# Optimization experiments

Hardware: AMD Instinct MI355X
Metric: run time of the kernel (lower is better)

## Reference

```python
import jax, jax.numpy as jnp
import numpy as np

N = 50000   # total nodes in batch
E = 640000  # directed edges
G = 64      # graphs in batch
D_IN = 128
D_H = 128
D_OUT = 10


def _glorot(key, shape):
    fan_in = shape[0]
    return jax.random.normal(key, shape, dtype=jnp.float32) / np.sqrt(fan_in)


def setup_inputs() -> dict:
    key = jax.random.key(0)
    ks = jax.random.split(key, 10)
    x = jax.random.normal(ks[0], (N, D_IN), dtype=jnp.float32)
    src = jax.random.randint(ks[1], (E,), 0, N, dtype=jnp.int32)
    dst = jax.random.randint(ks[2], (E,), 0, N, dtype=jnp.int32)
    batch = jnp.sort(jax.random.randint(ks[3], (N,), 0, G, dtype=jnp.int32))
    return {
        "x": x, "src": src, "dst": dst, "batch": batch,
        "W1": _glorot(ks[4], (D_IN, D_H)), "b1": jnp.zeros((D_H,), jnp.float32),
        "W2": _glorot(ks[5], (D_H, D_H)), "b2": jnp.zeros((D_H,), jnp.float32),
        "W3": _glorot(ks[6], (D_H, D_H)), "b3": jnp.zeros((D_H,), jnp.float32),
        "Wl": _glorot(ks[7], (D_H, D_OUT)), "bl": jnp.zeros((D_OUT,), jnp.float32),
    }


def gcn_conv(x, W, b, src, dst):
    """PyG GCNConv: add self-loops, symmetric deg^-1/2 normalization,
    linear transform, scatter-sum aggregation at dst, plus bias."""
    n = x.shape[0]
    loops = jnp.arange(n, dtype=src.dtype)
    s = jnp.concatenate([src, loops])  # [E+N]
    d = jnp.concatenate([dst, loops])
    deg = jax.ops.segment_sum(jnp.ones_like(d, dtype=x.dtype), d, num_segments=n)
    dinv = jnp.where(deg > 0, jax.lax.rsqrt(deg), 0.0)
    norm = dinv[s] * dinv[d]                        # [E+N]
    h = x @ W                                       # [N, D]
    out = jax.ops.segment_sum(h[s] * norm[:, None], d, num_segments=n)
    return out + b


def reference(x, src, dst, batch, W1, b1, W2, b2, W3, b3, Wl, bl):
    n = x.shape[0]
    h = jax.nn.relu(gcn_conv(x, W1, b1, src, dst))
    # dropout is a no-op in eval mode
    h = jax.nn.relu(gcn_conv(h, W2, b2, src, dst))
    h = gcn_conv(h, W3, b3, src, dst)
    # global_mean_pool over graph ids
    sums = jax.ops.segment_sum(h, batch, num_segments=G)            # [G, D]
    counts = jax.ops.segment_sum(jnp.ones((n,), h.dtype), batch, num_segments=G)
    pooled = sums / jnp.maximum(counts, 1.0)[:, None]
    logits = pooled @ Wl + bl                                       # [G, D_OUT]
    return jax.nn.log_softmax(logits, axis=1)
```

## Files before the change

kernel.cpp:

```cpp
#include <hip/hip_runtime.h>


constexpr int D = 128;
constexpr int DOUT = 10;
constexpr int PSPLIT = 8;
constexpr int BSH = 3;
constexpr int BCAP = 192;
constexpr int CPAD = 16;

using short8  = __attribute__((ext_vector_type(8))) short;
using float4v = __attribute__((ext_vector_type(4))) float;
using f32x2   = __attribute__((ext_vector_type(2))) float;

__device__ __forceinline__ ushort f2bf(float f) {
  uint u = __float_as_uint(f);
  return (ushort)((u + 0x7fffu + ((u >> 16) & 1u)) >> 16);
}
__device__ __forceinline__ float bfhi(uint u) { return __uint_as_float(u & 0xffff0000u); }


__global__ void init_kernel(int* __restrict__ bcnt, int total) {
  int i = blockIdx.x * blockDim.x + threadIdx.x;
  if (i < total) bcnt[i] = 0;
}

__global__ void binfill_kernel(const int* __restrict__ src, const int* __restrict__ dst,
    int* __restrict__ bcnt, uint* __restrict__ buck, int e) {
  int i = blockIdx.x * blockDim.x + threadIdx.x;
  if (i >= e) return;
  int d = dst[i], s = src[i];
  int b = d >> BSH;
  int pos = atomicAdd(&bcnt[b * CPAD], 1);
  if (pos < BCAP)
    buck[(size_t)b * BCAP + pos] = (uint)s | ((uint)(d & ((1 << BSH) - 1)) << 16);
}

__global__ __launch_bounds__(256) void countb_kernel(const uint* __restrict__ buck,
    const int* __restrict__ bcnt, int* __restrict__ cnt, float* __restrict__ dinv,
    int* __restrict__ bsum, int n) {
  __shared__ int lc[256];
  const int base = blockIdx.x * 256;
  const int m = min(256, n - base);
  lc[threadIdx.x] = 0;
  __syncthreads();
  const int b0 = base >> BSH;
  #pragma unroll
  for (int bb = 0; bb < (256 >> BSH); ++bb) {
    int b = b0 + bb;
    if ((b << BSH) >= n) break;
    int c = min(bcnt[b * CPAD], BCAP);
    for (int i = threadIdx.x; i < c; i += 256)
      atomicAdd(&lc[(bb << BSH) + (int)(buck[(size_t)b * BCAP + i] >> 16)], 1);
  }
  __syncthreads();
  int v = lc[threadIdx.x];
  if ((int)threadIdx.x < m) {
    cnt[base + threadIdx.x] = v;
    dinv[base + threadIdx.x] = rsqrtf((float)(v + 1));
  }
  __shared__ int sd[256];
  sd[threadIdx.x] = ((int)threadIdx.x < m) ? v : 0;
  __syncthreads();
  for (int off = 128; off > 0; off >>= 1) {
    if (threadIdx.x < (unsigned)off) sd[threadIdx.x] += sd[threadIdx.x + off];
    __syncthreads();
  }
  if (threadIdx.x == 0) bsum[blockIdx.x] = sd[0];
}

__global__ __launch_bounds__(1024) void scan2_kernel(const int* __restrict__ bsum,
    int* __restrict__ boff, int nb, int* __restrict__ rowptr, int n) {
  __shared__ int sd[1024];
  int v = ((int)threadIdx.x < nb) ? bsum[threadIdx.x] : 0;
  sd[threadIdx.x] = v;
  __syncthreads();
  for (int off = 1; off < 1024; off <<= 1) {
    int t = (threadIdx.x >= (unsigned)off) ? sd[threadIdx.x - off] : 0;
    __syncthreads();
    sd[threadIdx.x] += t;
    __syncthreads();
  }
  if ((int)threadIdx.x < nb) boff[threadIdx.x] = sd[threadIdx.x] - v;
  if ((int)threadIdx.x == nb - 1) rowptr[n] = sd[threadIdx.x];
}

__global__ __launch_bounds__(256) void scatter_kernel(const uint* __restrict__ buck,
    const int* __restrict__ bcnt, const int* __restrict__ cnt,
    const int* __restrict__ boff, int* __restrict__ rowptr,
    const float* __restrict__ dinv, uint* __restrict__ epk, int n) {
  __shared__ int sd[256];
  __shared__ int lcur[256];
  const int base = blockIdx.x * 256;
  const int i = base + (int)threadIdx.x;
  int v = (i < n) ? cnt[i] : 0;
  sd[threadIdx.x] = v;
  __syncthreads();
  for (int off = 1; off < 256; off <<= 1) {
    int t = (threadIdx.x >= (unsigned)off) ? sd[threadIdx.x - off] : 0;
    __syncthreads();
    sd[threadIdx.x] += t;
    __syncthreads();
  }
  int rp = boff[blockIdx.x] + sd[threadIdx.x] - v;
  if (i < n) {
    rowptr[i] = rp;
    lcur[threadIdx.x] = rp;
  }
  __syncthreads();
  const int b0 = base >> BSH;
  #pragma unroll
  for (int bb = 0; bb < (256 >> BSH); ++bb) {
    int b = b0 + bb;
    if ((b << BSH) >= n) break;
    int c = min(bcnt[b * CPAD], BCAP);
    for (int j = threadIdx.x; j < c; j += 256) {
      uint rec = buck[(size_t)b * BCAP + j];
      int dl = (int)(rec >> 16);
      int s = (int)(rec & 0xffffu);
      int d = (b << BSH) + dl;
      int slot = atomicAdd(&lcur[(bb << BSH) + dl], 1);
      epk[slot] = (uint)s | ((uint)f2bf(dinv[s] * dinv[d]) << 16);
    }
  }
}

__global__ __launch_bounds__(256) void prepw_kernel(const float* __restrict__ W1,
    const float* __restrict__ W2, const float* __restrict__ W3, ushort* __restrict__ Wp) {
  const float* W = (blockIdx.y == 0) ? W1 : (blockIdx.y == 1) ? W2 : W3;
  ushort* Wpo = Wp + (size_t)blockIdx.y * 2048 * 8;
  int idx = blockIdx.x * 256 + threadIdx.x;
  int cf = idx >> 8, kk = (idx >> 6) & 3, lane = idx & 63;
  int k0 = kk * 32 + (lane >> 4) * 8;
  int c = cf * 16 + (lane & 15);
  uint p[4];
  #pragma unroll
  for (int h = 0; h < 4; ++h) {
    ushort lo = f2bf(W[(k0 + 2 * h) * D + c]);
    ushort hi = f2bf(W[(k0 + 2 * h + 1) * D + c]);
    p[h] = (uint)lo | ((uint)hi << 16);
  }
  uint4 w = make_uint4(p[0], p[1], p[2], p[3]);
  *(uint4*)(Wpo + idx * 8) = w;
}

__global__ __launch_bounds__(256) void gemm_mfma(const float* __restrict__ Ain,
    const ushort* __restrict__ Wp, uchar* __restrict__ out, int n) {
  __shared__ ushort wl[2048 * 8];
  const int tid = threadIdx.x;
  #pragma unroll
  for (int i = 0; i < 8; ++i) {
    int idx = tid + i * 256;
    *(uint4*)(&wl[idx * 8]) = *(const uint4*)(Wp + idx * 8);
  }
  __syncthreads();
  const int w = tid >> 6, lane = tid & 63;
  const int row0 = blockIdx.x * 64 + w * 16;
  int arow = row0 + (lane & 15);
  if (arow >= n) arow = n - 1;

  short8 a[4];
  const float* abase = Ain + (size_t)arow * D + ((lane >> 4) * 8);
  #pragma unroll
  for (int kk = 0; kk < 4; ++kk) {
    float4 f0 = *(const float4*)(abase + kk * 32);
    float4 f1 = *(const float4*)(abase + kk * 32 + 4);
    short8 v;
    v[0] = (short)f2bf(f0.x); v[1] = (short)f2bf(f0.y);
    v[2] = (short)f2bf(f0.z); v[3] = (short)f2bf(f0.w);
    v[4] = (short)f2bf(f1.x); v[5] = (short)f2bf(f1.y);
    v[6] = (short)f2bf(f1.z); v[7] = (short)f2bf(f1.w);
    a[kk] = v;
  }

  float4v acc[8] = {};
  #pragma unroll
  for (int kk = 0; kk < 4; ++kk) {
    #pragma unroll
    for (int cf = 0; cf < 8; ++cf) {
      short8 b = *(const short8*)(&wl[((cf * 4 + kk) * 64 + lane) * 8]);
      acc[cf] = __builtin_amdgcn_mfma_f32_16x16x32_bf16(a[kk], b, acc[cf], 0, 0, 0);
    }
  }
  const int crow = row0 + (lane >> 4) * 4;
  const int ccol = lane & 15;
  #pragma unroll
  for (int cf = 0; cf < 8; ++cf) {
    #pragma unroll
    for (int r = 0; r < 4; ++r) {
      if (crow + r < n) {
        int enc = __builtin_amdgcn_cvt_pk_fp8_f32(acc[cf][r], acc[cf][r], 0, false);
        out[(size_t)(crow + r) * D + cf * 16 + ccol] = (uchar)(enc & 0xff);
      }
    }
  }
}

__device__ __forceinline__ void agg_node(const uchar* __restrict__ h8,
    const int* __restrict__ rowptr, const uint* __restrict__ epk,
    const float* __restrict__ dinv, const float* __restrict__ bias,
    int node, int sub, int li, int relu,
    float& a0, float& a1, float& a2, float& a3) {
  const int beg = rowptr[node], end = rowptr[node + 1];
  a0 = a1 = a2 = a3 = 0.f;
  for (int e = beg; e < end; e += 16) {
    uint mm[8], rr[8];
    #pragma unroll
    for (int k = 0; k < 8; ++k)
      mm[k] = epk[min(e + 2 * k + sub, end - 1)];
    #pragma unroll
    for (int k = 0; k < 8; ++k)
      rr[k] = *(const uint*)(h8 + (size_t)(mm[k] & 0xffffu) * D + li * 4);
    #pragma unroll
    for (int k = 0; k < 8; ++k) {
      float wk = (e + 2 * k + sub < end) ? bfhi(mm[k]) : 0.f;
      f32x2 pa = __builtin_amdgcn_cvt_pk_f32_fp8(rr[k], false);
      f32x2 pb = __builtin_amdgcn_cvt_pk_f32_fp8(rr[k], true);
      a0 += pa[0] * wk;
      a1 += pa[1] * wk;
      a2 += pb[0] * wk;
      a3 += pb[1] * wk;
    }
  }
  a0 += __shfl_xor(a0, 32);
  a1 += __shfl_xor(a1, 32);
  a2 += __shfl_xor(a2, 32);
  a3 += __shfl_xor(a3, 32);
  const float di = dinv[node];
  const float dsq = di * di;
  uint sv = *(const uint*)(h8 + (size_t)node * D + li * 4);
  f32x2 sa = __builtin_amdgcn_cvt_pk_f32_fp8(sv, false);
  f32x2 sb = __builtin_amdgcn_cvt_pk_f32_fp8(sv, true);
  a0 += sa[0] * dsq;
  a1 += sa[1] * dsq;
  a2 += sb[0] * dsq;
  a3 += sb[1] * dsq;
  float4 bv = *(const float4*)(bias + li * 4);
  a0 += bv.x; a1 += bv.y; a2 += bv.z; a3 += bv.w;
  if (relu) {
    a0 = fmaxf(a0, 0.f); a1 = fmaxf(a1, 0.f);
    a2 = fmaxf(a2, 0.f); a3 = fmaxf(a3, 0.f);
  }
}

__global__ __launch_bounds__(256) void aggemm_kernel(const uchar* __restrict__ h8,
    const int* __restrict__ rowptr, const uint* __restrict__ epk,
    const float* __restrict__ dinv, const float* __restrict__ bias,
    const ushort* __restrict__ Wp, uchar* __restrict__ out8, int n) {
  __shared__ ushort At[16][136];
  const int wv = (int)(threadIdx.x >> 6);
  const int lane = (int)(threadIdx.x & 63);
  const int sub = lane >> 5;
  const int li = lane & 31;
  const int node0 = blockIdx.x * 16;
  #pragma unroll
  for (int t = 0; t < 4; ++t) {
    const int row = wv * 4 + t;
    const int node = node0 + row;
    if (node < n) {
      float a0, a1, a2, a3;
      agg_node(h8, rowptr, epk, dinv, bias, node, sub, li, 1, a0, a1, a2, a3);
      if (sub == 0) {
        uint2 pk;
        pk.x = (uint)f2bf(a0) | ((uint)f2bf(a1) << 16);
        pk.y = (uint)f2bf(a2) | ((uint)f2bf(a3) << 16);
        *(uint2*)(&At[row][li * 4]) = pk;
      }
    } else if (sub == 0) {
      *(uint2*)(&At[row][li * 4]) = make_uint2(0, 0);
    }
  }
  __syncthreads();
  const int r = lane & 15;
  const int koff = (lane >> 4) * 8;
  short8 a[4];
  #pragma unroll
  for (int kk = 0; kk < 4; ++kk)
    a[kk] = *(const short8*)(&At[r][koff + kk * 32]);
  const int crow = node0 + (lane >> 4) * 4;
  const int ccol = lane & 15;
  #pragma unroll
  for (int cc = 0; cc < 2; ++cc) {
    const int cf = wv * 2 + cc;
    float4v acc = {};
    #pragma unroll
    for (int kk = 0; kk < 4; ++kk) {
      short8 b = *(const short8*)(Wp + (size_t)((cf * 4 + kk) * 64 + lane) * 8);
      acc = __builtin_amdgcn_mfma_f32_16x16x32_bf16(a[kk], b, acc, 0, 0, 0);
    }
    #pragma unroll
    for (int r2 = 0; r2 < 4; ++r2) {
      if (crow + r2 < n) {
        int enc = __builtin_amdgcn_cvt_pk_fp8_f32(acc[r2], acc[r2], 0, false);
        out8[(size_t)(crow + r2) * D + cf * 16 + ccol] = (uchar)(enc & 0xff);
      }
    }
  }
}

__global__ __launch_bounds__(256) void agg_kernel(const uchar* __restrict__ h8,
    const int* __restrict__ rowptr, const uint* __restrict__ epk,
    const float* __restrict__ dinv, const float* __restrict__ bias,
    uchar* __restrict__ out8, int n, int relu) {
  int node = (int)((blockIdx.x * blockDim.x + threadIdx.x) >> 6);
  if (node >= n) return;
  const int lane = threadIdx.x & 63;
  const int sub = lane >> 5;
  const int li = lane & 31;
  float a0, a1, a2, a3;
  agg_node(h8, rowptr, epk, dinv, bias, node, sub, li, relu, a0, a1, a2, a3);
  if (sub == 0) {
    int enc = __builtin_amdgcn_cvt_pk_fp8_f32(a0, a1, 0, false);
    enc = __builtin_amdgcn_cvt_pk_fp8_f32(a2, a3, enc, true);
    *(uint*)(out8 + (size_t)node * D + li * 4) = (uint)enc;
  }
}

__global__ __launch_bounds__(256) void pool1_kernel(const uchar* __restrict__ act8,
    const int* __restrict__ batch, float* __restrict__ pp, int n) {
  const int g = blockIdx.x;
  const int sp = blockIdx.y;
  int lo = 0, hi = n;
  while (lo < hi) { int mid = (lo + hi) >> 1; if (batch[mid] < g) lo = mid + 1; else hi = mid; }
  const int start = lo;
  hi = n;
  while (lo < hi) { int mid = (lo + hi) >> 1; if (batch[mid] <= g) lo = mid + 1; else hi = mid; }
  const int end = lo;
  const int len = end - start;
  const int per = (len + PSPLIT - 1) / PSPLIT;
  const int i0 = start + sp * per;
  const int i1 = min(i0 + per, end);

  const int rt = threadIdx.x >> 4;
  const int ds = threadIdx.x & 15;
  float acc[8] = {};
  for (int i = i0 + rt; i < i1; i += 16) {
    uint2 v = *(const uint2*)(act8 + (size_t)i * D + ds * 8);
    f32x2 p0 = __builtin_amdgcn_cvt_pk_f32_fp8(v.x, false);
    f32x2 p1 = __builtin_amdgcn_cvt_pk_f32_fp8(v.x, true);
    f32x2 p2 = __builtin_amdgcn_cvt_pk_f32_fp8(v.y, false);
    f32x2 p3 = __builtin_amdgcn_cvt_pk_f32_fp8(v.y, true);
    acc[0] += p0[0]; acc[1] += p0[1]; acc[2] += p1[0]; acc[3] += p1[1];
    acc[4] += p2[0]; acc[5] += p2[1]; acc[6] += p3[0]; acc[7] += p3[1];
  }
  __shared__ float sd[256][8];
  #pragma unroll
  for (int e2 = 0; e2 < 8; ++e2) sd[threadIdx.x][e2] = acc[e2];
  __syncthreads();
  if (threadIdx.x < 128) {
    int d = threadIdx.x;
    int slice = d >> 3, e2 = d & 7;
    float s = 0.f;
    #pragma unroll
    for (int k = 0; k < 16; ++k) s += sd[k * 16 + slice][e2];
    pp[((size_t)g * PSPLIT + sp) * D + d] = s;
  }
}

__global__ __launch_bounds__(640) void head_kernel(const float* __restrict__ pp,
    const int* __restrict__ batch, const float* __restrict__ Wl,
    const float* __restrict__ bl, float* __restrict__ out, int n, int g) {
  __shared__ float pooled[64 * D];
  __shared__ float cnts[64];
  __shared__ float lg[64][DOUT];
  const int tid = threadIdx.x;
  if (tid < g) {
    int gg = tid;
    int lo = 0, hi = n;
    while (lo < hi) { int mid = (lo + hi) >> 1; if (batch[mid] < gg) lo = mid + 1; else hi = mid; }
    int start = lo;
    hi = n;
    while (lo < hi) { int mid = (lo + hi) >> 1; if (batch[mid] <= gg) lo = mid + 1; else hi = mid; }
    cnts[gg] = fmaxf((float)(lo - start), 1.f);
  }
  __syncthreads();
  for (int idx = tid; idx < g * D; idx += 640) {
    int gg = idx >> 7, d = idx & 127;
    float s = 0.f;
    #pragma unroll
    for (int sp = 0; sp < PSPLIT; ++sp) s += pp[((size_t)gg * PSPLIT + sp) * D + d];
    pooled[idx] = s / cnts[gg];
  }
  __syncthreads();
  int gi = tid / DOUT, o = tid % DOUT;
  if (gi < g) {
    float acc = bl[o];
    for (int d = 0; d < D; ++d) acc += pooled[gi * D + d] * Wl[d * DOUT + o];
    lg[gi][o] = acc;
  }
  __syncthreads();
  if (gi < g) {
    float m = -1e30f;
    for (int j = 0; j < DOUT; ++j) m = fmaxf(m, lg[gi][j]);
    float s = 0.f;
    for (int j = 0; j < DOUT; ++j) s += expf(lg[gi][j] - m);
    out[gi * DOUT + o] = lg[gi][o] - m - logf(s);
  }
}


extern "C" void kernel_launch(void* const* d_in, const int* in_sizes, int n_in,
                              void* d_out, int out_size, void* d_ws, size_t ws_size,
                              hipStream_t stream) {
  const float* x   = (const float*)d_in[0];
  const int* src   = (const int*)d_in[1];
  const int* dst   = (const int*)d_in[2];
  const int* batch = (const int*)d_in[3];
  const float* W1  = (const float*)d_in[4];
  const float* b1  = (const float*)d_in[5];
  const float* W2  = (const float*)d_in[6];
  const float* b2  = (const float*)d_in[7];
  const float* W3  = (const float*)d_in[8];
  const float* b3  = (const float*)d_in[9];
  const float* Wl  = (const float*)d_in[10];
  const float* bl  = (const float*)d_in[11];
  float* out = (float*)d_out;

  const int n = in_sizes[0] / D;
  const int e = in_sizes[1];
  const int g = out_size / DOUT;

  char* p = (char*)d_ws;
  auto alloc = [&](size_t bytes) {
    char* r = p;
    p += (bytes + 255) & ~(size_t)255;
    return r;
  };
  const int nb = (n + 255) / 256;
  const int NB = (n + (1 << BSH) - 1) >> BSH;
  int* cnt      = (int*)alloc((size_t)n * 4);
  int* rowptr   = (int*)alloc((size_t)(n + 1) * 4);
  float* dinv   = (float*)alloc((size_t)n * 4);
  int* bsum     = (int*)alloc((size_t)nb * 4);
  int* boff     = (int*)alloc((size_t)nb * 4);
  int* bcnt     = (int*)alloc((size_t)NB * CPAD * 4);
  uint* buck    = (uint*)alloc((size_t)NB * BCAP * 4);
  uint* epk     = (uint*)alloc((size_t)e * 4);
  ushort* Wp    = (ushort*)alloc(3 * 2048 * 16);
  uchar* tmpA   = (uchar*)alloc((size_t)n * D);
  uchar* tmpB   = (uchar*)alloc((size_t)n * D);
  float* pp     = (float*)alloc((size_t)g * PSPLIT * D * 4);
  (void)ws_size;

  const int B = 256;
  const int gridE = (e + B - 1) / B;

  init_kernel<<<(NB * CPAD + B - 1) / B, B, 0, stream>>>(bcnt, NB * CPAD);
  binfill_kernel<<<gridE, B, 0, stream>>>(src, dst, bcnt, buck, e);
  countb_kernel<<<nb, B, 0, stream>>>(buck, bcnt, cnt, dinv, bsum, n);
  scan2_kernel<<<1, 1024, 0, stream>>>(bsum, boff, nb, rowptr, n);
  scatter_kernel<<<nb, B, 0, stream>>>(buck, bcnt, cnt, boff, rowptr, dinv, epk, n);
  prepw_kernel<<<dim3(8, 3), B, 0, stream>>>(W1, W2, W3, Wp);

  const int gemmGrid = (n + 63) / 64;
  const int fuseGrid = (n + 15) / 16;
  const int aggGrid = (n * 64 + B - 1) / B;

  gemm_mfma<<<gemmGrid, B, 0, stream>>>(x, Wp, tmpA, n);
  aggemm_kernel<<<fuseGrid, B, 0, stream>>>(tmpA, rowptr, epk, dinv, b1,
                                            Wp + 2048 * 8, tmpB, n);
  aggemm_kernel<<<fuseGrid, B, 0, stream>>>(tmpB, rowptr, epk, dinv, b2,
                                            Wp + 2 * 2048 * 8, tmpA, n);
  agg_kernel<<<aggGrid, B, 0, stream>>>(tmpA, rowptr, epk, dinv, b3, tmpB, n, 0);

  pool1_kernel<<<dim3(g, PSPLIT), B, 0, stream>>>(tmpB, batch, pp, n);
  head_kernel<<<1, 640, 0, stream>>>(pp, batch, Wl, bl, out, n, g);
}
```

Baseline: 188.0 us.

## Fuse layer-1 GEMM into edge binning kernel via heterogeneous block ranges

Merges the edge bucketing kernel and the first-layer MFMA GEMM into one launch: the first gridE blocks bin edges and the remaining blocks compute x@W1, with each GEMM block converting W1 to packed bf16 in shared memory itself. This removes a separate kernel launch and lets the independent GEMM overlap with the atomic-heavy binning. The prepw kernel now handles only W2 and W3. In exchange, every GEMM block repacks W1 redundantly from global memory, and the binning blocks reserve the 32KB shared array, which can limit their occupancy.

Result: no change. 187.6 us (-0.2%).

```diff
diff --git a/kernel.cpp b/kernel.cpp
--- a/kernel.cpp
+++ b/kernel.cpp
@@ -24,15 +24,79 @@
   if (i < total) bcnt[i] = 0;
 }
 
-__global__ void binfill_kernel(const int* __restrict__ src, const int* __restrict__ dst,
-    int* __restrict__ bcnt, uint* __restrict__ buck, int e) {
-  int i = blockIdx.x * blockDim.x + threadIdx.x;
-  if (i >= e) return;
-  int d = dst[i], s = src[i];
-  int b = d >> BSH;
-  int pos = atomicAdd(&bcnt[b * CPAD], 1);
-  if (pos < BCAP)
-    buck[(size_t)b * BCAP + pos] = (uint)s | ((uint)(d & ((1 << BSH) - 1)) << 16);
+__global__ __launch_bounds__(256) void binfill_gemm_kernel(
+    const int* __restrict__ src, const int* __restrict__ dst,
+    int* __restrict__ bcnt, uint* __restrict__ buck, int e, int gridE,
+    const float* __restrict__ x, const float* __restrict__ W1,
+    uchar* __restrict__ out8, int n) {
+  __shared__ ushort wl[2048 * 8];
+  const int tid = threadIdx.x;
+  if ((int)blockIdx.x < gridE) {
+    int i = blockIdx.x * 256 + tid;
+    if (i < e) {
+      int d = dst[i], s = src[i];
+      int b = d >> BSH;
+      int pos = atomicAdd(&bcnt[b * CPAD], 1);
+      if (pos < BCAP)
+        buck[(size_t)b * BCAP + pos] = (uint)s | ((uint)(d & ((1 << BSH) - 1)) << 16);
+    }
+    return;
+  }
+  const int bid = (int)blockIdx.x - gridE;
+  for (int t = tid; t < 2048; t += 256) {
+    int cf = t >> 8, kk = (t >> 6) & 3, lane2 = t & 63;
+    int k0 = kk * 32 + (lane2 >> 4) * 8;
+    int c = cf * 16 + (lane2 & 15);
+    uint p[4];
+    #pragma unroll
+    for (int h = 0; h < 4; ++h) {
+      ushort lo = f2bf(W1[(k0 + 2 * h) * D + c]);
+      ushort hi = f2bf(W1[(k0 + 2 * h + 1) * D + c]);
+      p[h] = (uint)lo | ((uint)hi << 16);
+    }
+    *(uint4*)(&wl[t * 8]) = make_uint4(p[0], p[1], p[2], p[3]);
+  }
+  __syncthreads();
+  const int w = tid >> 6, lane = tid & 63;
+  const int row0 = bid * 64 + w * 16;
+  int arow = row0 + (lane & 15);
+  if (arow >= n) arow = n - 1;
+
+  short8 a[4];
+  const float* abase = x + (size_t)arow * D + ((lane >> 4) * 8);
+  #pragma unroll
+  for (int kk = 0; kk < 4; ++kk) {
+    float4 f0 = *(const float4*)(abase + kk * 32);
+    float4 f1 = *(const float4*)(abase + kk * 32 + 4);
+    short8 v;
+    v[0] = (short)f2bf(f0.x); v[1] = (short)f2bf(f0.y);
+    v[2] = (short)f2bf(f0.z); v[3] = (short)f2bf(f0.w);
+    v[4] = (short)f2bf(f1.x); v[5] = (short)f2bf(f1.y);
+    v[6] = (short)f2bf(f1.z); v[7] = (short)f2bf(f1.w);
+    a[kk] = v;
+  }
+
+  float4v acc[8] = {};
+  #pragma unroll
+  for (int kk = 0; kk < 4; ++kk) {
+    #pragma unroll
+    for (int cf = 0; cf < 8; ++cf) {
+      short8 b = *(const short8*)(&wl[((cf * 4 + kk) * 64 + lane) * 8]);
+      acc[cf] = __builtin_amdgcn_mfma_f32_16x16x32_bf16(a[kk], b, acc[cf], 0, 0, 0);
+    }
+  }
+  const int crow = row0 + (lane >> 4) * 4;
+  const int ccol = lane & 15;
+  #pragma unroll
+  for (int cf = 0; cf < 8; ++cf) {
+    #pragma unroll
+    for (int r = 0; r < 4; ++r) {
+      if (crow + r < n) {
+        int enc = __builtin_amdgcn_cvt_pk_fp8_f32(acc[cf][r], acc[cf][r], 0, false);
+        out8[(size_t)(crow + r) * D + cf * 16 + ccol] = (uchar)(enc & 0xff);
+      }
+    }
+  }
 }
 
 __global__ __launch_bounds__(256) void countb_kernel(const uint* __restrict__ buck,
@@ -124,9 +188,9 @@
   }
 }
 
-__global__ __launch_bounds__(256) void prepw_kernel(const float* __restrict__ W1,
-    const float* __restrict__ W2, const float* __restrict__ W3, ushort* __restrict__ Wp) {
-  const float* W = (blockIdx.y == 0) ? W1 : (blockIdx.y == 1) ? W2 : W3;
+__global__ __launch_bounds__(256) void prepw_kernel(const float* __restrict__ W2,
+    const float* __restrict__ W3, ushort* __restrict__ Wp) {
+  const float* W = (blockIdx.y == 0) ? W2 : W3;
   ushort* Wpo = Wp + (size_t)blockIdx.y * 2048 * 8;
   int idx = blockIdx.x * 256 + threadIdx.x;
   int cf = idx >> 8, kk = (idx >> 6) & 3, lane = idx & 63;
@@ -141,58 +205,6 @@
   }
   uint4 w = make_uint4(p[0], p[1], p[2], p[3]);
   *(uint4*)(Wpo + idx * 8) = w;
-}
-
-__global__ __launch_bounds__(256) void gemm_mfma(const float* __restrict__ Ain,
-    const ushort* __restrict__ Wp, uchar* __restrict__ out, int n) {
-  __shared__ ushort wl[2048 * 8];
-  const int tid = threadIdx.x;
-  #pragma unroll
-  for (int i = 0; i < 8; ++i) {
-    int idx = tid + i * 256;
-    *(uint4*)(&wl[idx * 8]) = *(const uint4*)(Wp + idx * 8);
-  }
-  __syncthreads();
-  const int w = tid >> 6, lane = tid & 63;
-  const int row0 = blockIdx.x * 64 + w * 16;
-  int arow = row0 + (lane & 15);
-  if (arow >= n) arow = n - 1;
-
-  short8 a[4];
-  const float* abase = Ain + (size_t)arow * D + ((lane >> 4) * 8);
-  #pragma unroll
-  for (int kk = 0; kk < 4; ++kk) {
-    float4 f0 = *(const float4*)(abase + kk * 32);
-    float4 f1 = *(const float4*)(abase + kk * 32 + 4);
-    short8 v;
-    v[0] = (short)f2bf(f0.x); v[1] = (short)f2bf(f0.y);
-    v[2] = (short)f2bf(f0.z); v[3] = (short)f2bf(f0.w);
-    v[4] = (short)f2bf(f1.x); v[5] = (short)f2bf(f1.y);
-    v[6] = (short)f2bf(f1.z); v[7] = (short)f2bf(f1.w);
-    a[kk] = v;
-  }
-
-  float4v acc[8] = {};
-  #pragma unroll
-  for (int kk = 0; kk < 4; ++kk) {
-    #pragma unroll
-    for (int cf = 0; cf < 8; ++cf) {
-      short8 b = *(const short8*)(&wl[((cf * 4 + kk) * 64 + lane) * 8]);
-      acc[cf] = __builtin_amdgcn_mfma_f32_16x16x32_bf16(a[kk], b, acc[cf], 0, 0, 0);
-    }
-  }
-  const int crow = row0 + (lane >> 4) * 4;
-  const int ccol = lane & 15;
-  #pragma unroll
-  for (int cf = 0; cf < 8; ++cf) {
-    #pragma unroll
-    for (int r = 0; r < 4; ++r) {
-      if (crow + r < n) {
-        int enc = __builtin_amdgcn_cvt_pk_fp8_f32(acc[cf][r], acc[cf][r], 0, false);
-        out[(size_t)(crow + r) * D + cf * 16 + ccol] = (uchar)(enc & 0xff);
-      }
-    }
-  }
 }
 
 __device__ __forceinline__ void agg_node(const uchar* __restrict__ h8,
@@ -435,7 +447,7 @@
   int* bcnt     = (int*)alloc((size_t)NB * CPAD * 4);
   uint* buck    = (uint*)alloc((size_t)NB * BCAP * 4);
   uint* epk     = (uint*)alloc((size_t)e * 4);
-  ushort* Wp    = (ushort*)alloc(3 * 2048 * 16);
+  ushort* Wp    = (ushort*)alloc(2 * 2048 * 16);
   uchar* tmpA   = (uchar*)alloc((size_t)n * D);
   uchar* tmpB   = (uchar*)alloc((size_t)n * D);
   float* pp     = (float*)alloc((size_t)g * PSPLIT * D * 4);
@@ -443,23 +455,23 @@
 
   const int B = 256;
   const int gridE = (e + B - 1) / B;
+  const int gemmGrid = (n + 63) / 64;
 
   init_kernel<<<(NB * CPAD + B - 1) / B, B, 0, stream>>>(bcnt, NB * CPAD);
-  binfill_kernel<<<gridE, B, 0, stream>>>(src, dst, bcnt, buck, e);
+  binfill_gemm_kernel<<<gridE + gemmGrid, B, 0, stream>>>(
+      src, dst, bcnt, buck, e, gridE, x, W1, tmpA, n);
   countb_kernel<<<nb, B, 0, stream>>>(buck, bcnt, cnt, dinv, bsum, n);
   scan2_kernel<<<1, 1024, 0, stream>>>(bsum, boff, nb, rowptr, n);
   scatter_kernel<<<nb, B, 0, stream>>>(buck, bcnt, cnt, boff, rowptr, dinv, epk, n);
-  prepw_kernel<<<dim3(8, 3), B, 0, stream>>>(W1, W2, W3, Wp);
-
-  const int gemmGrid = (n + 63) / 64;
+  prepw_kernel<<<dim3(8, 2), B, 0, stream>>>(W2, W3, Wp);
+
   const int fuseGrid = (n + 15) / 16;
   const int aggGrid = (n * 64 + B - 1) / B;
 
-  gemm_mfma<<<gemmGrid, B, 0, stream>>>(x, Wp, tmpA, n);
   aggemm_kernel<<<fuseGrid, B, 0, stream>>>(tmpA, rowptr, epk, dinv, b1,
-                                            Wp + 2048 * 8, tmpB, n);
+                                            Wp, tmpB, n);
   aggemm_kernel<<<fuseGrid, B, 0, stream>>>(tmpB, rowptr, epk, dinv, b2,
-                                            Wp + 2 * 2048 * 8, tmpA, n);
+                                            Wp + 2048 * 8, tmpA, n);
   agg_kernel<<<aggGrid, B, 0, stream>>>(tmpA, rowptr, epk, dinv, b3, tmpB, n, 0);
 
   pool1_kernel<<<dim3(g, PSPLIT), B, 0, stream>>>(tmpB, batch, pp, n);
```
